# Kernel tuning notes

Hardware: AMD Instinct MI355X
Metric: run time of the kernel (lower is better)

## Reference

```python
import jax, jax.numpy as jnp
import numpy as np

MIN_R = 0.05
MAX_R = 0.3
K = 16  # num_neighbors


def setup_inputs() -> dict:
    key = jax.random.key(0)
    k1, k2, k3 = jax.random.split(key, 3)
    B, N, M, C = 4, 16384, 2048, 64
    points = jax.random.uniform(k1, (B, N, 3), dtype=jnp.float32)
    features = jax.random.normal(k2, (B, N, C), dtype=jnp.float32)
    center_indices = jax.random.randint(k3, (B, M), 0, N)
    return {"points": points, "features": features, "center_indices": center_indices}


def reference(points, features, center_indices):
    B, N, _ = points.shape
    # gather center coordinates: [B, M, 3]
    centers = jnp.take_along_axis(points, center_indices[:, :, None], axis=1)
    # pairwise distances [B, M, N] (direct diff form, matching torch.norm)
    diff = points[:, None, :, :] - centers[:, :, None, :]
    dist = jnp.sqrt(jnp.sum(diff * diff, axis=-1))
    # density from count of points within min_radius
    init_counts = jnp.sum(dist < MIN_R, axis=-1, keepdims=True).astype(jnp.float32)
    density = init_counts / (4.0 / 3.0 * np.pi * MIN_R ** 3 + 1e-8)
    density_max = jnp.max(density) + 1e-8
    radii = MIN_R + (MAX_R - MIN_R) * (1.0 - density / density_max)  # [B, M, 1]
    # mask out points outside per-center radius, then k smallest distances
    dist = jnp.where(dist < radii, dist, 1e10)
    _, knn_indices = jax.lax.top_k(-dist, K)  # [B, M, K]
    knn_indices = jnp.clip(knn_indices, 0, N - 1)
    # gather neighbor features: [B, M, K, C]
    neighbor_features = jax.vmap(lambda f, idx: f[idx])(features, knn_indices)
    return neighbor_features
```

## Files before the change

### kernel.cpp

```cpp
#include <hip/hip_runtime.h>
#include <stdint.h>

#define BB 4
#define NN 16384
#define MM 2048
#define CC 64
#define KK 16
#define WAVES 4
#define G 16
#define NC (G * G * G)
#define SCAP 128
#define CAP 512
#define ZERO_INTS (4 + BB * NC)

typedef unsigned long long u64;
typedef unsigned int u32;
typedef unsigned short u16;
typedef unsigned char u8;

__device__ __forceinline__ float axdist(float c, int cell) {
  const float lo = (float)cell * (1.0f / (float)G);
  const float hi = (float)(cell + 1) * (1.0f / (float)G);
  float d = 0.0f;
  if (c < lo) d = lo - c;
  else if (c > hi) d = c - hi;
  return d;
}

#define LGKM_WAIT() __asm__ volatile("s_waitcnt lgkmcnt(0)" ::: "memory")

__device__ __forceinline__ u64 wave_min_u64(u64 v) {
#pragma unroll
  for (int off = 32; off > 0; off >>= 1) {
    u64 o = __shfl_xor(v, off, 64);
    v = (o < v) ? o : v;
  }
  return v;
}

__global__ __launch_bounds__(256) void zero_ws_kernel(int* __restrict__ w) {
  const int i = blockIdx.x * 256 + threadIdx.x;
  if (i < ZERO_INTS) w[i] = 0;
}

__global__ __launch_bounds__(256) void cell_count_kernel(
    const float* __restrict__ pts, int* __restrict__ cell_cnt) {
  const int tid = blockIdx.x * 256 + threadIdx.x;
  const int b = tid >> 14, i = tid & (NN - 1);
  const float* p = pts + (size_t)b * NN * 3 + (size_t)i * 3;
  int ix = (int)(p[0] * (float)G); ix = ix < 0 ? 0 : (ix > G - 1 ? G - 1 : ix);
  int iy = (int)(p[1] * (float)G); iy = iy < 0 ? 0 : (iy > G - 1 ? G - 1 : iy);
  int iz = (int)(p[2] * (float)G); iz = iz < 0 ? 0 : (iz > G - 1 ? G - 1 : iz);
  atomicAdd(&cell_cnt[b * NC + (iz * G + iy) * G + ix], 1);
}

__global__ __launch_bounds__(256) void cell_scan_kernel(
    const int* __restrict__ cell_cnt, int* __restrict__ cell_start,
    int* __restrict__ cursor) {
  __shared__ u32 wsum[WAVES];
  const int b = blockIdx.x;
  const int* cnt = cell_cnt + b * NC;
  int* st = cell_start + b * (NC + 1);
  int* cur = cursor + b * NC;
  const int base = threadIdx.x * 16;
  const int lane = threadIdx.x & 63;
  const int wave = threadIdx.x >> 6;
  int loc[16];
  int s = 0;
#pragma unroll
  for (int i = 0; i < 16; ++i) { loc[i] = s; s += cnt[base + i]; }
  u32 inc = (u32)s;
#pragma unroll
  for (int off = 1; off < 64; off <<= 1) {
    u32 t = __shfl_up(inc, off, 64);
    if (lane >= off) inc += t;
  }
  if (lane == 63) wsum[wave] = inc;
  __syncthreads();
  u32 woff = 0;
#pragma unroll
  for (int w = 0; w < WAVES; ++w) woff += (w < wave) ? wsum[w] : 0u;
  const u32 off = woff + inc - (u32)s;
#pragma unroll
  for (int i = 0; i < 16; ++i) {
    const int v = (int)(off + (u32)loc[i]);
    st[base + i] = v;
    cur[base + i] = v;
  }
  if (threadIdx.x == 0) st[NC] = NN;
}

__global__ __launch_bounds__(256) void cell_fill_kernel(
    const float* __restrict__ pts, int* __restrict__ cursor,
    float4* __restrict__ sorted) {
  const int tid = blockIdx.x * 256 + threadIdx.x;
  const int b = tid >> 14, i = tid & (NN - 1);
  const float* p = pts + (size_t)b * NN * 3 + (size_t)i * 3;
  const float x = p[0], y = p[1], z = p[2];
  int ix = (int)(x * (float)G); ix = ix < 0 ? 0 : (ix > G - 1 ? G - 1 : ix);
  int iy = (int)(y * (float)G); iy = iy < 0 ? 0 : (iy > G - 1 ? G - 1 : iy);
  int iz = (int)(z * (float)G); iz = iz < 0 ? 0 : (iz > G - 1 ? G - 1 : iz);
  const int cell = (iz * G + iy) * G + ix;
  const int pos = atomicAdd(&cursor[b * NC + cell], 1);
  sorted[(size_t)b * NN + pos] = make_float4(x, y, z, __uint_as_float((u32)i));
}

__global__ __launch_bounds__(256) void grid_count_kernel(
    const float* __restrict__ points, const int* __restrict__ cidx,
    const int* __restrict__ cell_start, const float4* __restrict__ sorted,
    int* __restrict__ counts, int* __restrict__ maxcnt) {
#pragma clang fp contract(off)
  const int sub = threadIdx.x & 15;
  const int grp = threadIdx.x >> 4;
  const int center = blockIdx.x * 16 + grp;
  const int b = center >> 11;
  const float* pb = points + (size_t)b * (NN * 3);
  const int ci = cidx[center];
  const float ccx = pb[ci * 3 + 0], ccy = pb[ci * 3 + 1], ccz = pb[ci * 3 + 2];
  const float R0 = 0.05f;
  const float rc = R0 * 1.0001f + 1e-6f;
  const float rc2 = rc * rc;
  const int lox = max(0, (int)floorf((ccx - rc) * (float)G));
  const int hix = min(G - 1, (int)floorf((ccx + rc) * (float)G));
  const int loy = max(0, (int)floorf((ccy - rc) * (float)G));
  const int hiy = min(G - 1, (int)floorf((ccy + rc) * (float)G));
  const int loz = max(0, (int)floorf((ccz - rc) * (float)G));
  const int hiz = min(G - 1, (int)floorf((ccz + rc) * (float)G));
  const int cs0 = b * (NC + 1);
  const float4* sp = sorted + (size_t)b * NN;
  int cnt = 0;
  for (int zc = loz; zc <= hiz; ++zc) {
    const float dz0 = axdist(ccz, zc);
    for (int yc = loy; yc <= hiy; ++yc) {
      const float dy0 = axdist(ccy, yc);
      const float dd = dy0 * dy0 + dz0 * dz0;
      if (dd >= rc2) continue;
      const float half = sqrtf(rc2 - dd) * 1.0001f + 1e-6f;
      const int xl = max(lox, (int)floorf((ccx - half) * (float)G));
      const int xh = min(hix, (int)floorf((ccx + half) * (float)G));
      if (xl > xh) continue;
      const int row = cs0 + (zc * G + yc) * G;
      const int s0 = cell_start[row + xl];
      const int e0 = cell_start[row + xh + 1];
      for (int p = s0 + sub; p < e0; p += 16) {
        const float4 pt = sp[p];
        const float dx = pt.x - ccx, dy = pt.y - ccy, dz = pt.z - ccz;
        const float d = sqrtf((dx * dx + dy * dy) + dz * dz);
        cnt += (d < R0) ? 1 : 0;
      }
    }
  }
#pragma unroll
  for (int off = 8; off > 0; off >>= 1) cnt += __shfl_xor(cnt, off, 16);
  if (sub == 0) {
    counts[center] = cnt;
    atomicMax(maxcnt, cnt);
  }
}

#define WALK(BODY)                                                   \
  {                                                                  \
    int ri = 0;                                                      \
    for (u32 w = (u32)lane; w < T; w += 64) {                        \
      while (rowC[ri + 1] <= w) ++ri;                                \
      const int p = (int)rowS[ri] + (int)(w - rowC[ri]);             \
      const float4 pt = sp[p];                                       \
      const float dx = pt.x - ccx, dy = pt.y - ccy, dz = pt.z - ccz; \
      const float d = sqrtf((dx * dx + dy * dy) + dz * dz);          \
      BODY                                                           \
    }                                                                \
  }

__global__ __launch_bounds__(256, 6) void grid_topk_kernel(
    const float* __restrict__ points, const float* __restrict__ features,
    const int* __restrict__ cidx, const int* __restrict__ counts,
    const int* __restrict__ maxcnt, const int* __restrict__ cell_start,
    const float4* __restrict__ sorted, float* __restrict__ out) {
#pragma clang fp contract(off)
  __shared__ u16 cand_s[WAVES][CAP];
  __shared__ u8  candb_s[WAVES][CAP];
  __shared__ u64 surv_s[WAVES][SCAP + 2];
  __shared__ u32 rowS_s[WAVES][128];
  __shared__ u32 rowC_s[WAVES][128];
  __shared__ u32 hist_s[WAVES][128];

  const int lane = threadIdx.x & 63;
  const int wave = threadIdx.x >> 6;
  const int center = blockIdx.x * WAVES + wave;
  const int b = center >> 11;
  u16* cand = cand_s[wave];
  u8*  candb = candb_s[wave];
  u64* surv = surv_s[wave];
  u32* rowS = rowS_s[wave];
  u32* rowC = rowC_s[wave];
  u32* hist = hist_s[wave];
  const u64 lanemask = (((u64)1 << lane) - 1);

  const float* pb = points + (size_t)b * (NN * 3);
  const int ci = cidx[center];
  const float ccx = pb[ci * 3 + 0], ccy = pb[ci * 3 + 1], ccz = pb[ci * 3 + 2];

  const int cnt_c = counts[center];
  const float DENOM = (float)(4.0 / 3.0 * 3.141592653589793 * (0.05 * 0.05 * 0.05) + 1e-8);
  const float dens = (float)cnt_c / DENOM;
  const float dmax = (float)(*maxcnt) / DENOM + 1e-8f;
  const float r = 0.05f + 0.25f * (1.0f - dens / dmax);
  const int cs0 = b * (NC + 1);
  const float4* sp = sorted + (size_t)b * NN;

  const float tA = fminf(r, fmaxf(0.055f,
      0.05f * cbrtf(16.0f / fmaxf((float)cnt_c, 0.5f)) * 1.35f));

  u32 scnt = 0;

  for (int attempt = 0; attempt < 2; ++attempt) {
    const float t_eff = (attempt == 0) ? tA : r;
    const bool finals = (attempt == 1) || (tA >= r);
    const float rc = t_eff * 1.0001f + 1e-6f;
    const float rc2 = rc * rc;
    const float bs1 = 32.0f / t_eff;
    const float bs2 = 1024.0f / t_eff;

    const int lox = max(0, (int)floorf((ccx - rc) * (float)G));
    const int hix = min(G - 1, (int)floorf((ccx + rc) * (float)G));
    const int loy = max(0, (int)floorf((ccy - rc) * (float)G));
    const int hiy = min(G - 1, (int)floorf((ccy + rc) * (float)G));
    const int loz = max(0, (int)floorf((ccz - rc) * (float)G));
    const int hiz = min(G - 1, (int)floorf((ccz + rc) * (float)G));

    const int ny = hiy - loy + 1;
    const int nrows = ny * (hiz - loz + 1);
    u32 len0 = 0, len1 = 0, st0 = 0, st1 = 0;
#pragma unroll
    for (int half_i = 0; half_i < 2; ++half_i) {
      const int rr = lane + half_i * 64;
      u32 st = 0, len = 0;
      if (rr < nrows) {
        const int zz = rr / ny, yy = rr - zz * ny;
        const int zc = loz + zz, yc = loy + yy;
        const float dz0 = axdist(ccz, zc);
        const float dy0 = axdist(ccy, yc);
        const float dd = dy0 * dy0 + dz0 * dz0;
        if (dd < rc2) {
          const float half = sqrtf(rc2 - dd) * 1.0001f + 1e-6f;
          const int xl = max(lox, (int)floorf((ccx - half) * (float)G));
          const int xh = min(hix, (int)floorf((ccx + half) * (float)G));
          if (xl <= xh) {
            const int row = cs0 + (zc * G + yc) * G;
            const int s0 = cell_start[row + xl];
            const int e0 = cell_start[row + xh + 1];
            st = (u32)s0; len = (u32)(e0 - s0);
          }
        }
      }
      if (half_i == 0) { st0 = st; len0 = len; } else { st1 = st; len1 = len; }
    }
    u32 a = len0;
#pragma unroll
    for (int off = 1; off < 64; off <<= 1) {
      u32 t = __shfl_up(a, off, 64);
      if (lane >= off) a += t;
    }
    const u32 tot0 = __shfl(a, 63, 64);
    u32 bcum = len1;
#pragma unroll
    for (int off = 1; off < 64; off <<= 1) {
      u32 t = __shfl_up(bcum, off, 64);
      if (lane >= off) bcum += t;
    }
    const u32 T = tot0 + __shfl(bcum, 63, 64);
    rowS[lane] = st0;
    rowS[lane + 64] = st1;
    rowC[lane] = a - len0;
    rowC[lane + 64] = tot0 + bcum - len1;
    hist[lane] = 0;
    hist[lane + 64] = 0;
    LGKM_WAIT();

    u32 scn = 0;
    {
      int riA = 0, riB = 0;
      for (u32 w = (u32)lane; w < T; w += 128) {
        while (rowC[riA + 1] <= w) ++riA;
        const int pA = (int)rowS[riA] + (int)(w - rowC[riA]);
        const float4 ptA = sp[pA];
        const u32 w2 = w + 64;
        const bool hasB = (w2 < T);
        int pB = 0;
        float xB = 4e4f, yB = 4e4f, zB = 4e4f;
        if (hasB) {
          if (riB < riA) riB = riA;
          while (rowC[riB + 1] <= w2) ++riB;
          pB = (int)rowS[riB] + (int)(w2 - rowC[riB]);
          const float4 ptB = sp[pB];
          xB = ptB.x; yB = ptB.y; zB = ptB.z;
        }
        const float dxA = ptA.x - ccx, dyA = ptA.y - ccy, dzA = ptA.z - ccz;
        const float dA = sqrtf((dxA * dxA + dyA * dyA) + dzA * dzA);
        const float dxB = xB - ccx, dyB = yB - ccy, dzB = zB - ccz;
        const float dB = sqrtf((dxB * dxB + dyB * dyB) + dzB * dzB);
        const bool accA = dA < t_eff;
        const bool accB = hasB && (dB < t_eff);
        const u64 maskA = __ballot(accA);
        const u64 maskB = __ballot(accB);
        if (accA) {
          int bin = (int)(dA * bs1); bin = bin > 31 ? 31 : bin;
          atomicAdd(&hist[((lane & 3) << 5) + bin], 1u);
          const u32 pos = scn + (u32)__popcll(maskA & lanemask);
          if (pos < (u32)CAP) { cand[pos] = (u16)pA; candb[pos] = (u8)bin; }
        }
        const u32 cA = (u32)__popcll(maskA);
        if (accB) {
          int bin = (int)(dB * bs1); bin = bin > 31 ? 31 : bin;
          atomicAdd(&hist[((lane & 3) << 5) + bin], 1u);
          const u32 pos = scn + cA + (u32)__popcll(maskB & lanemask);
          if (pos < (u32)CAP) { cand[pos] = (u16)pB; candb[pos] = (u8)bin; }
        }
        scn += cA + (u32)__popcll(maskB);
      }
    }
    LGKM_WAIT();

    u32 incl = 0;
    if (lane < 32) incl = hist[lane] + hist[lane + 32] + hist[lane + 64] + hist[lane + 96];
#pragma unroll
    for (int off = 1; off < 32; off <<= 1) {
      u32 t = __shfl_up(incl, off, 32);
      if ((lane & 31) >= off) incl += t;
    }
    const u32 total = __shfl(incl, 31, 64);
    const bool overflow = total > (u32)CAP;

    if (total < (u32)KK) {
      if (!finals) continue;
      for (u32 i = lane; i < total; i += 64) {
        const float4 pt = sp[cand[i]];
        const float dx = pt.x - ccx, dy = pt.y - ccy, dz = pt.z - ccz;
        const float d = sqrtf((dx * dx + dy * dy) + dz * dz);
        surv[i] = ((u64)__float_as_uint(d) << 32) | __float_as_uint(pt.w);
      }
      scnt = total;
      LGKM_WAIT();
      break;
    }

    u64 bm = __ballot(lane < 32 && incl >= (u32)KK);
    const int b1 = (__ffsll(bm) - 1);
    const u32 cnt_b1 = __shfl(incl, b1, 64);
    const u32 pre = (b1 > 0) ? __shfl(incl, b1 - 1, 64) : 0u;

    int b2 = 31;
    const bool need2 = (pre + cnt_b1 > (u32)SCAP);
    if (need2) {
      hist[lane] = 0;
      hist[lane + 64] = 0;
      LGKM_WAIT();
      if (!overflow) {
        for (u32 i = lane; i < total; i += 64) {
          if ((int)candb[i] == b1) {
            const float4 pt = sp[cand[i]];
            const float dx = pt.x - ccx, dy = pt.y - ccy, dz = pt.z - ccz;
            const float d = sqrtf((dx * dx + dy * dy) + dz * dz);
            int o = (int)(d * bs2) - (b1 << 5);
            o = o < 0 ? 0 : (o > 31 ? 31 : o);
            atomicAdd(&hist[((lane & 3) << 5) + o], 1u);
          }
        }
      } else {
        WALK({
          if (d < t_eff) {
            int bin = (int)(d * bs1); bin = bin > 31 ? 31 : bin;
            if (bin == b1) {
              int o = (int)(d * bs2) - (b1 << 5);
              o = o < 0 ? 0 : (o > 31 ? 31 : o);
              atomicAdd(&hist[((lane & 3) << 5) + o], 1u);
            }
          }
        })
      }
      LGKM_WAIT();
      u32 incl2 = 0;
      if (lane < 32) incl2 = hist[lane] + hist[lane + 32] + hist[lane + 64] + hist[lane + 96];
#pragma unroll
      for (int off = 1; off < 32; off <<= 1) {
        u32 t = __shfl_up(incl2, off, 32);
        if ((lane & 31) >= off) incl2 += t;
      }
      const u32 target = (u32)KK - pre;
      u64 bm2 = __ballot(lane < 32 && incl2 >= target);
      b2 = bm2 ? (__ffsll(bm2) - 1) : 31;
    }

    u32 sc = 0;
    if (!overflow) {
      for (u32 i = lane; i < total; i += 64) {
        const int bin = (int)candb[i];
        bool acc2;
        float d = 0.0f;
        u32 pw = 0;
        if (!need2) {
          acc2 = (bin <= b1);
          if (acc2) {
            const float4 pt = sp[cand[i]];
            const float dx = pt.x - ccx, dy = pt.y - ccy, dz = pt.z - ccz;
            d = sqrtf((dx * dx + dy * dy) + dz * dz);
            pw = __float_as_uint(pt.w);
          }
        } else {
          acc2 = (bin < b1);
          if (bin == b1) {
            const float4 pt = sp[cand[i]];
            const float dx = pt.x - ccx, dy = pt.y - ccy, dz = pt.z - ccz;
            d = sqrtf((dx * dx + dy * dy) + dz * dz);
            pw = __float_as_uint(pt.w);
            int o = (int)(d * bs2) - (b1 << 5);
            o = o < 0 ? 0 : (o > 31 ? 31 : o);
            acc2 = (o <= b2);
          } else if (acc2) {
            const float4 pt = sp[cand[i]];
            const float dx = pt.x - ccx, dy = pt.y - ccy, dz = pt.z - ccz;
            d = sqrtf((dx * dx + dy * dy) + dz * dz);
            pw = __float_as_uint(pt.w);
          }
        }
        const u64 mask = __ballot(acc2);
        if (acc2) {
          const u32 pos = sc + (u32)__popcll(mask & lanemask);
          if (pos < (u32)SCAP)
            surv[pos] = ((u64)__float_as_uint(d) << 32) | pw;
        }
        sc += (u32)__popcll(mask);
      }
    } else {
      WALK({
        bool acc2 = false;
        if (d < t_eff) {
          int bin = (int)(d * bs1); bin = bin > 31 ? 31 : bin;
          if (!need2) acc2 = (bin <= b1);
          else {
            int o = (int)(d * bs2) - (b1 << 5);
            o = o < 0 ? 0 : (o > 31 ? 31 : o);
            acc2 = (bin < b1) || (bin == b1 && o <= b2);
          }
        }
        const u64 mask = __ballot(acc2);
        if (acc2) {
          const u32 pos = sc + (u32)__popcll(mask & lanemask);
          if (pos < (u32)SCAP)
            surv[pos] = ((u64)__float_as_uint(d) << 32) | __float_as_uint(pt.w);
        }
        sc += (u32)__popcll(mask);
      })
    }
    sc = (u32)__shfl((int)sc, 0, 64);
    scnt = sc > (u32)SCAP ? (u32)SCAP : sc;
    LGKM_WAIT();
    break;
  }

  if (scnt < (u32)KK) {
    for (int base = 0; base < NN && scnt < (u32)KK; base += 64) {
      const int i = base + lane;
      const float x = pb[i * 3 + 0], y = pb[i * 3 + 1], z = pb[i * 3 + 2];
      const float dx = x - ccx, dy = y - ccy, dz = z - ccz;
      const float d = sqrtf((dx * dx + dy * dy) + dz * dz);
      u64 m = __ballot(!(d < r));
      while (m && scnt < (u32)KK) {
        const int t = __ffsll(m) - 1;
        m &= m - 1;
        if (lane == 0)
          surv[scnt] = ((u64)__float_as_uint(1e10f) << 32) | (u32)(base + t);
        scnt++;
      }
    }
    LGKM_WAIT();
  }

  {
    const u64 k0 = (lane < (int)scnt) ? surv[lane] : ~0ULL;
    const u64 k1 = (lane + 64 < (int)scnt) ? surv[lane + 64] : ~0ULL;
    u32 rank0 = 0, rank1 = 0;
    for (u32 j = 0; j < scnt; ++j) {
      const u64 kj = surv[j];
      rank0 += (kj < k0) ? 1u : 0u;
      rank1 += (kj < k1) ? 1u : 0u;
    }
    if (lane < (int)scnt && rank0 < (u32)KK) rowS[rank0] = (u32)(k0 & 0xffffffffULL);
    if (lane + 64 < (int)scnt && rank1 < (u32)KK) rowS[rank1] = (u32)(k1 & 0xffffffffULL);
    LGKM_WAIT();
  }

  const float* fb = features + (size_t)b * NN * CC;
  float* ob = out + (size_t)center * KK * CC;
  const int ch4 = (lane & 15) * 4;
  const int ksub = lane >> 4;
#pragma unroll
  for (int kq = 0; kq < 4; ++kq) {
    const int k = kq * 4 + ksub;
    const int nk = (int)rowS[k];
    const float4 v = *(const float4*)(fb + (size_t)nk * CC + ch4);
    *(float4*)(ob + (size_t)k * CC + ch4) = v;
  }
}

#define CH 4096
#define NCHUNK (NN / CH)

__global__ __launch_bounds__(256) void fb_count_kernel(
    const float* __restrict__ points, const int* __restrict__ cidx,
    int* __restrict__ counts, int* __restrict__ maxcnt) {
#pragma clang fp contract(off)
  __shared__ float s[CH * 3];
  const int lane = threadIdx.x & 63;
  const int wave = threadIdx.x >> 6;
  const int center = blockIdx.x * WAVES + wave;
  const int b = center >> 11;
  const float* pb = points + (size_t)b * (NN * 3);
  const int ci = cidx[center];
  const float cx = pb[ci * 3 + 0], cy = pb[ci * 3 + 1], cz = pb[ci * 3 + 2];
  int cnt = 0;
  for (int c = 0; c < NCHUNK; ++c) {
    __syncthreads();
    const float4* src = (const float4*)(pb + (size_t)c * CH * 3);
    float4* dst = (float4*)s;
    for (int i = threadIdx.x; i < CH * 3 / 4; i += 256) dst[i] = src[i];
    __syncthreads();
    for (int j = 0; j < CH / 64; ++j) {
      const int p = j * 64 + lane;
      const float dx = s[p * 3 + 0] - cx;
      const float dy = s[p * 3 + 1] - cy;
      const float dz = s[p * 3 + 2] - cz;
      const float d = sqrtf((dx * dx + dy * dy) + dz * dz);
      cnt += (d < 0.05f) ? 1 : 0;
    }
  }
#pragma unroll
  for (int off = 32; off > 0; off >>= 1) cnt += __shfl_xor(cnt, off, 64);
  if (lane == 0) { counts[center] = cnt; atomicMax(maxcnt, cnt); }
}

__global__ __launch_bounds__(256) void fb_topk_kernel(
    const float* __restrict__ points, const float* __restrict__ features,
    const int* __restrict__ cidx, const int* __restrict__ counts,
    const int* __restrict__ maxcnt, float* __restrict__ out) {
#pragma clang fp contract(off)
  __shared__ float s[CH * 3];
  const int lane = threadIdx.x & 63;
  const int wave = threadIdx.x >> 6;
  const int center = blockIdx.x * WAVES + wave;
  const int b = center >> 11;
  const float* pb = points + (size_t)b * (NN * 3);
  const int ci = cidx[center];
  const float cx = pb[ci * 3 + 0], cy = pb[ci * 3 + 1], cz = pb[ci * 3 + 2];
  const float DENOM = (float)(4.0 / 3.0 * 3.141592653589793 * (0.05 * 0.05 * 0.05) + 1e-8);
  const float dens = (float)counts[center] / DENOM;
  const float dmax = (float)(*maxcnt) / DENOM + 1e-8f;
  const float r = 0.05f + 0.25f * (1.0f - dens / dmax);
  u64 kb[KK];
#pragma unroll
  for (int i = 0; i < KK; ++i) kb[i] = ~0ULL;
  u64 worst = ~0ULL, T = ~0ULL;
  for (int c = 0; c < NCHUNK; ++c) {
    __syncthreads();
    const float4* src = (const float4*)(pb + (size_t)c * CH * 3);
    float4* dst = (float4*)s;
    for (int i = threadIdx.x; i < CH * 3 / 4; i += 256) dst[i] = src[i];
    __syncthreads();
    const int nbase = c * CH;
    for (int j = 0; j < CH / 64; ++j) {
      const int p = j * 64 + lane;
      const float dx = s[p * 3 + 0] - cx;
      const float dy = s[p * 3 + 1] - cy;
      const float dz = s[p * 3 + 2] - cz;
      const float d = sqrtf((dx * dx + dy * dy) + dz * dz);
      const float dm = (d < r) ? d : 1e10f;
      const u64 key = ((u64)__float_as_uint(dm) << 32) | (unsigned)(nbase + p);
      if (key < T && key < worst) {
        u64 cc = key;
#pragma unroll
        for (int i = 0; i < KK; ++i) {
          const bool lt = kb[i] < cc;
          const u64 lo = lt ? kb[i] : cc;
          const u64 hi = lt ? cc : kb[i];
          kb[i] = lo; cc = hi;
        }
        worst = kb[KK - 1];
      }
    }
    if (c == 0) {
      u64 t[KK];
#pragma unroll
      for (int i = 0; i < KK; ++i) t[i] = kb[i];
      u64 g = 0;
#pragma unroll
      for (int k = 0; k < KK; ++k) {
        g = wave_min_u64(t[0]);
        if (t[0] == g) {
#pragma unroll
          for (int i = 0; i < KK - 1; ++i) t[i] = t[i + 1];
          t[KK - 1] = ~0ULL;
        }
      }
      T = g;
    }
  }
  int knn[KK];
#pragma unroll
  for (int k = 0; k < KK; ++k) {
    const u64 g = wave_min_u64(kb[0]);
    if (kb[0] == g) {
#pragma unroll
      for (int i = 0; i < KK - 1; ++i) kb[i] = kb[i + 1];
      kb[KK - 1] = ~0ULL;
    }
    knn[k] = (int)(unsigned)(g & 0xffffffffULL);
  }
  const float* fb = features + (size_t)b * NN * CC;
  float* ob = out + (size_t)center * KK * CC;
#pragma unroll
  for (int k = 0; k < KK; ++k) ob[k * CC + lane] = fb[(size_t)knn[k] * CC + lane];
}

extern "C" void kernel_launch(void* const* d_in, const int* in_sizes, int n_in,
                              void* d_out, int out_size, void* d_ws, size_t ws_size,
                              hipStream_t stream) {
  const float* points   = (const float*)d_in[0];
  const float* features = (const float*)d_in[1];
  const int*   cidx     = (const int*)d_in[2];
  float* out = (float*)d_out;

  char* w = (char*)d_ws;
  const size_t off_cellcnt = 16;
  const size_t off_cursor  = off_cellcnt + (size_t)BB * NC * 4;
  const size_t off_counts  = off_cursor + (size_t)BB * NC * 4;
  const size_t off_cstart  = off_counts + (size_t)BB * MM * 4;
  const size_t off_sorted  = (off_cstart + (size_t)BB * (NC + 1) * 4 + 15) & ~(size_t)15;
  const size_t need        = off_sorted + (size_t)BB * NN * 16;

  int* maxcnt = (int*)w;
  dim3 block(256);

  if (ws_size >= need) {
    int* cell_cnt   = (int*)(w + off_cellcnt);
    int* cursor     = (int*)(w + off_cursor);
    int* counts     = (int*)(w + off_counts);
    int* cell_start = (int*)(w + off_cstart);
    float4* sorted  = (float4*)(w + off_sorted);

    zero_ws_kernel<<<dim3((ZERO_INTS + 255) / 256), block, 0, stream>>>((int*)w);
    cell_count_kernel<<<dim3(BB * NN / 256), block, 0, stream>>>(points, cell_cnt);
    cell_scan_kernel<<<dim3(BB), block, 0, stream>>>(cell_cnt, cell_start, cursor);
    cell_fill_kernel<<<dim3(BB * NN / 256), block, 0, stream>>>(points, cursor, sorted);
    grid_count_kernel<<<dim3(BB * MM / 16), block, 0, stream>>>(
        points, cidx, cell_start, sorted, counts, maxcnt);
    grid_topk_kernel<<<dim3(BB * MM / WAVES), block, 0, stream>>>(
        points, features, cidx, counts, maxcnt, cell_start, sorted, out);
  } else {
    int* counts = (int*)w + 16;
    hipMemsetAsync(maxcnt, 0, sizeof(int), stream);
    fb_count_kernel<<<dim3(BB * MM / WAVES), block, 0, stream>>>(points, cidx, counts, maxcnt);
    fb_topk_kernel<<<dim3(BB * MM / WAVES), block, 0, stream>>>(points, features, cidx, counts, maxcnt, out);
  }
}
```

Baseline: 71.28 us.

## Fuse grid build stages into one persistent kernel with global barriers

Merges the cell count, scan, fill and density-count kernels into a single 512-block kernel separated by software grid barriers built on an atomic counter in the workspace. This removes three kernel launches and the gaps between them. In exchange it depends on all 512 blocks being resident at the same time, which deadlocks if they are not, and the spin barriers add their own latency.

```diff
diff --git a/kernel.cpp b/kernel.cpp
--- a/kernel.cpp
+++ b/kernel.cpp
@@ -11,6 +11,7 @@
 #define NC (G * G * G)
 #define SCAP 128
 #define CAP 512
+#define NBLK 512
 #define ZERO_INTS (4 + BB * NC)
 
 typedef unsigned long long u64;
@@ -38,123 +39,138 @@
   return v;
 }
 
+__device__ __forceinline__ void gbar(int* ctr, int target) {
+  __syncthreads();
+  if (threadIdx.x == 0) {
+    __threadfence();
+    __hip_atomic_fetch_add(ctr, 1, __ATOMIC_ACQ_REL, __HIP_MEMORY_SCOPE_AGENT);
+    while (__hip_atomic_load(ctr, __ATOMIC_ACQUIRE, __HIP_MEMORY_SCOPE_AGENT) < target) {
+      __builtin_amdgcn_s_sleep(2);
+    }
+    __threadfence();
+  }
+  __syncthreads();
+}
+
 __global__ __launch_bounds__(256) void zero_ws_kernel(int* __restrict__ w) {
   const int i = blockIdx.x * 256 + threadIdx.x;
   if (i < ZERO_INTS) w[i] = 0;
 }
 
-__global__ __launch_bounds__(256) void cell_count_kernel(
-    const float* __restrict__ pts, int* __restrict__ cell_cnt) {
+__global__ __launch_bounds__(256) void build_kernel(
+    const float* __restrict__ pts, const int* __restrict__ cidx,
+    int* __restrict__ bar, int* __restrict__ cell_cnt,
+    int* __restrict__ cell_start, int* __restrict__ cursor,
+    float4* __restrict__ sorted, int* __restrict__ counts,
+    int* __restrict__ maxcnt) {
+#pragma clang fp contract(off)
+  __shared__ u32 wsum[WAVES];
   const int tid = blockIdx.x * 256 + threadIdx.x;
-  const int b = tid >> 14, i = tid & (NN - 1);
-  const float* p = pts + (size_t)b * NN * 3 + (size_t)i * 3;
-  int ix = (int)(p[0] * (float)G); ix = ix < 0 ? 0 : (ix > G - 1 ? G - 1 : ix);
-  int iy = (int)(p[1] * (float)G); iy = iy < 0 ? 0 : (iy > G - 1 ? G - 1 : iy);
-  int iz = (int)(p[2] * (float)G); iz = iz < 0 ? 0 : (iz > G - 1 ? G - 1 : iz);
-  atomicAdd(&cell_cnt[b * NC + (iz * G + iy) * G + ix], 1);
-}
-
-__global__ __launch_bounds__(256) void cell_scan_kernel(
-    const int* __restrict__ cell_cnt, int* __restrict__ cell_start,
-    int* __restrict__ cursor) {
-  __shared__ u32 wsum[WAVES];
-  const int b = blockIdx.x;
-  const int* cnt = cell_cnt + b * NC;
-  int* st = cell_start + b * (NC + 1);
-  int* cur = cursor + b * NC;
-  const int base = threadIdx.x * 16;
-  const int lane = threadIdx.x & 63;
-  const int wave = threadIdx.x >> 6;
-  int loc[16];
-  int s = 0;
-#pragma unroll
-  for (int i = 0; i < 16; ++i) { loc[i] = s; s += cnt[base + i]; }
-  u32 inc = (u32)s;
-#pragma unroll
-  for (int off = 1; off < 64; off <<= 1) {
-    u32 t = __shfl_up(inc, off, 64);
-    if (lane >= off) inc += t;
-  }
-  if (lane == 63) wsum[wave] = inc;
-  __syncthreads();
-  u32 woff = 0;
-#pragma unroll
-  for (int w = 0; w < WAVES; ++w) woff += (w < wave) ? wsum[w] : 0u;
-  const u32 off = woff + inc - (u32)s;
-#pragma unroll
-  for (int i = 0; i < 16; ++i) {
-    const int v = (int)(off + (u32)loc[i]);
-    st[base + i] = v;
-    cur[base + i] = v;
-  }
-  if (threadIdx.x == 0) st[NC] = NN;
-}
-
-__global__ __launch_bounds__(256) void cell_fill_kernel(
-    const float* __restrict__ pts, int* __restrict__ cursor,
-    float4* __restrict__ sorted) {
-  const int tid = blockIdx.x * 256 + threadIdx.x;
-  const int b = tid >> 14, i = tid & (NN - 1);
-  const float* p = pts + (size_t)b * NN * 3 + (size_t)i * 3;
-  const float x = p[0], y = p[1], z = p[2];
-  int ix = (int)(x * (float)G); ix = ix < 0 ? 0 : (ix > G - 1 ? G - 1 : ix);
-  int iy = (int)(y * (float)G); iy = iy < 0 ? 0 : (iy > G - 1 ? G - 1 : iy);
-  int iz = (int)(z * (float)G); iz = iz < 0 ? 0 : (iz > G - 1 ? G - 1 : iz);
-  const int cell = (iz * G + iy) * G + ix;
-  const int pos = atomicAdd(&cursor[b * NC + cell], 1);
-  sorted[(size_t)b * NN + pos] = make_float4(x, y, z, __uint_as_float((u32)i));
-}
-
-__global__ __launch_bounds__(256) void grid_count_kernel(
-    const float* __restrict__ points, const int* __restrict__ cidx,
-    const int* __restrict__ cell_start, const float4* __restrict__ sorted,
-    int* __restrict__ counts, int* __restrict__ maxcnt) {
-#pragma clang fp contract(off)
-  const int sub = threadIdx.x & 15;
-  const int grp = threadIdx.x >> 4;
-  const int center = blockIdx.x * 16 + grp;
-  const int b = center >> 11;
-  const float* pb = points + (size_t)b * (NN * 3);
-  const int ci = cidx[center];
-  const float ccx = pb[ci * 3 + 0], ccy = pb[ci * 3 + 1], ccz = pb[ci * 3 + 2];
-  const float R0 = 0.05f;
-  const float rc = R0 * 1.0001f + 1e-6f;
-  const float rc2 = rc * rc;
-  const int lox = max(0, (int)floorf((ccx - rc) * (float)G));
-  const int hix = min(G - 1, (int)floorf((ccx + rc) * (float)G));
-  const int loy = max(0, (int)floorf((ccy - rc) * (float)G));
-  const int hiy = min(G - 1, (int)floorf((ccy + rc) * (float)G));
-  const int loz = max(0, (int)floorf((ccz - rc) * (float)G));
-  const int hiz = min(G - 1, (int)floorf((ccz + rc) * (float)G));
-  const int cs0 = b * (NC + 1);
-  const float4* sp = sorted + (size_t)b * NN;
-  int cnt = 0;
-  for (int zc = loz; zc <= hiz; ++zc) {
-    const float dz0 = axdist(ccz, zc);
-    for (int yc = loy; yc <= hiy; ++yc) {
-      const float dy0 = axdist(ccy, yc);
-      const float dd = dy0 * dy0 + dz0 * dz0;
-      if (dd >= rc2) continue;
-      const float half = sqrtf(rc2 - dd) * 1.0001f + 1e-6f;
-      const int xl = max(lox, (int)floorf((ccx - half) * (float)G));
-      const int xh = min(hix, (int)floorf((ccx + half) * (float)G));
-      if (xl > xh) continue;
-      const int row = cs0 + (zc * G + yc) * G;
-      const int s0 = cell_start[row + xl];
-      const int e0 = cell_start[row + xh + 1];
-      for (int p = s0 + sub; p < e0; p += 16) {
-        const float4 pt = sp[p];
-        const float dx = pt.x - ccx, dy = pt.y - ccy, dz = pt.z - ccz;
-        const float d = sqrtf((dx * dx + dy * dy) + dz * dz);
-        cnt += (d < R0) ? 1 : 0;
-      }
-    }
-  }
-#pragma unroll
-  for (int off = 8; off > 0; off >>= 1) cnt += __shfl_xor(cnt, off, 16);
-  if (sub == 0) {
-    counts[center] = cnt;
-    atomicMax(maxcnt, cnt);
+
+  if (tid < BB * NN) {
+    const int b = tid >> 14, i = tid & (NN - 1);
+    const float* p = pts + (size_t)b * NN * 3 + (size_t)i * 3;
+    int ix = (int)(p[0] * (float)G); ix = ix < 0 ? 0 : (ix > G - 1 ? G - 1 : ix);
+    int iy = (int)(p[1] * (float)G); iy = iy < 0 ? 0 : (iy > G - 1 ? G - 1 : iy);
+    int iz = (int)(p[2] * (float)G); iz = iz < 0 ? 0 : (iz > G - 1 ? G - 1 : iz);
+    atomicAdd(&cell_cnt[b * NC + (iz * G + iy) * G + ix], 1);
+  }
+  gbar(bar, NBLK);
+
+  if (blockIdx.x < BB) {
+    const int b = blockIdx.x;
+    const int* cnt = cell_cnt + b * NC;
+    int* st = cell_start + b * (NC + 1);
+    int* cur = cursor + b * NC;
+    const int base = threadIdx.x * 16;
+    const int lane = threadIdx.x & 63;
+    const int wave = threadIdx.x >> 6;
+    int loc[16];
+    int s = 0;
+#pragma unroll
+    for (int i = 0; i < 16; ++i) { loc[i] = s; s += cnt[base + i]; }
+    u32 inc = (u32)s;
+#pragma unroll
+    for (int off = 1; off < 64; off <<= 1) {
+      u32 t = __shfl_up(inc, off, 64);
+      if (lane >= off) inc += t;
+    }
+    if (lane == 63) wsum[wave] = inc;
+    __syncthreads();
+    u32 woff = 0;
+#pragma unroll
+    for (int w = 0; w < WAVES; ++w) woff += (w < wave) ? wsum[w] : 0u;
+    const u32 off = woff + inc - (u32)s;
+#pragma unroll
+    for (int i = 0; i < 16; ++i) {
+      const int v = (int)(off + (u32)loc[i]);
+      st[base + i] = v;
+      cur[base + i] = v;
+    }
+    if (threadIdx.x == 0) st[NC] = NN;
+  }
+  gbar(bar, 2 * NBLK);
+
+  if (tid < BB * NN) {
+    const int b = tid >> 14, i = tid & (NN - 1);
+    const float* p = pts + (size_t)b * NN * 3 + (size_t)i * 3;
+    const float x = p[0], y = p[1], z = p[2];
+    int ix = (int)(x * (float)G); ix = ix < 0 ? 0 : (ix > G - 1 ? G - 1 : ix);
+    int iy = (int)(y * (float)G); iy = iy < 0 ? 0 : (iy > G - 1 ? G - 1 : iy);
+    int iz = (int)(z * (float)G); iz = iz < 0 ? 0 : (iz > G - 1 ? G - 1 : iz);
+    const int cell = (iz * G + iy) * G + ix;
+    const int pos = atomicAdd(&cursor[b * NC + cell], 1);
+    sorted[(size_t)b * NN + pos] = make_float4(x, y, z, __uint_as_float((u32)i));
+  }
+  gbar(bar, 3 * NBLK);
+
+  {
+    const int sub = threadIdx.x & 15;
+    const int grp = threadIdx.x >> 4;
+    const int center = blockIdx.x * 16 + grp;
+    const int b = center >> 11;
+    const float* pb = pts + (size_t)b * (NN * 3);
+    const int ci = cidx[center];
+    const float ccx = pb[ci * 3 + 0], ccy = pb[ci * 3 + 1], ccz = pb[ci * 3 + 2];
+    const float R0 = 0.05f;
+    const float rc = R0 * 1.0001f + 1e-6f;
+    const float rc2 = rc * rc;
+    const int lox = max(0, (int)floorf((ccx - rc) * (float)G));
+    const int hix = min(G - 1, (int)floorf((ccx + rc) * (float)G));
+    const int loy = max(0, (int)floorf((ccy - rc) * (float)G));
+    const int hiy = min(G - 1, (int)floorf((ccy + rc) * (float)G));
+    const int loz = max(0, (int)floorf((ccz - rc) * (float)G));
+    const int hiz = min(G - 1, (int)floorf((ccz + rc) * (float)G));
+    const int cs0 = b * (NC + 1);
+    const float4* sp = sorted + (size_t)b * NN;
+    int cnt = 0;
+    for (int zc = loz; zc <= hiz; ++zc) {
+      const float dz0 = axdist(ccz, zc);
+      for (int yc = loy; yc <= hiy; ++yc) {
+        const float dy0 = axdist(ccy, yc);
+        const float dd = dy0 * dy0 + dz0 * dz0;
+        if (dd >= rc2) continue;
+        const float half = sqrtf(rc2 - dd) * 1.0001f + 1e-6f;
+        const int xl = max(lox, (int)floorf((ccx - half) * (float)G));
+        const int xh = min(hix, (int)floorf((ccx + half) * (float)G));
+        if (xl > xh) continue;
+        const int row = cs0 + (zc * G + yc) * G;
+        const int s0 = cell_start[row + xl];
+        const int e0 = cell_start[row + xh + 1];
+        for (int p = s0 + sub; p < e0; p += 16) {
+          const float4 pt = sp[p];
+          const float dx = pt.x - ccx, dy = pt.y - ccy, dz = pt.z - ccz;
+          const float d = sqrtf((dx * dx + dy * dy) + dz * dz);
+          cnt += (d < R0) ? 1 : 0;
+        }
+      }
+    }
+#pragma unroll
+    for (int off = 8; off > 0; off >>= 1) cnt += __shfl_xor(cnt, off, 16);
+    if (sub == 0) {
+      counts[center] = cnt;
+      atomicMax(maxcnt, cnt);
+    }
   }
 }
 
@@ -638,6 +654,7 @@
   const size_t need        = off_sorted + (size_t)BB * NN * 16;
 
   int* maxcnt = (int*)w;
+  int* bar    = (int*)w + 1;
   dim3 block(256);
 
   if (ws_size >= need) {
@@ -648,11 +665,8 @@
     float4* sorted  = (float4*)(w + off_sorted);
 
     zero_ws_kernel<<<dim3((ZERO_INTS + 255) / 256), block, 0, stream>>>((int*)w);
-    cell_count_kernel<<<dim3(BB * NN / 256), block, 0, stream>>>(points, cell_cnt);
-    cell_scan_kernel<<<dim3(BB), block, 0, stream>>>(cell_cnt, cell_start, cursor);
-    cell_fill_kernel<<<dim3(BB * NN / 256), block, 0, stream>>>(points, cursor, sorted);
-    grid_count_kernel<<<dim3(BB * MM / 16), block, 0, stream>>>(
-        points, cidx, cell_start, sorted, counts, maxcnt);
+    build_kernel<<<dim3(NBLK), block, 0, stream>>>(
+        points, cidx, bar, cell_cnt, cell_start, cursor, sorted, counts, maxcnt);
     grid_topk_kernel<<<dim3(BB * MM / WAVES), block, 0, stream>>>(
         points, features, cidx, counts, maxcnt, cell_start, sorted, out);
   } else {
```

After: 205.3 us. 188% more time.
